# Kernel optimization log

Hardware: AMD Instinct MI355X
Metric: run time of the kernel (lower is better)

Reference implementation:

```python
import jax, jax.numpy as jnp
import numpy as np

N_NODES = 100000
N_EDGES = 1600000
IN_DIM = 128
HID = 64
OUT = 1


def setup_inputs() -> dict:
    key = jax.random.key(0)
    ks = jax.random.split(key, 8)
    x = jax.random.normal(ks[0], (N_NODES, IN_DIM), dtype=jnp.float32)
    edge_src = jax.random.randint(ks[1], (N_EDGES,), 0, N_NODES)
    edge_dst = jax.random.randint(ks[2], (N_EDGES,), 0, N_NODES)
    edge_weight = jax.random.uniform(ks[3], (N_EDGES,), dtype=jnp.float32)
    W1 = jax.random.normal(ks[4], (IN_DIM, HID), dtype=jnp.float32) / np.sqrt(IN_DIM)
    b1 = jnp.zeros((HID,), dtype=jnp.float32)
    W2 = jax.random.normal(ks[5], (HID, OUT), dtype=jnp.float32) / np.sqrt(HID)
    b2 = jnp.zeros((OUT,), dtype=jnp.float32)
    return {"x": x, "edge_src": edge_src, "edge_dst": edge_dst,
            "edge_weight": edge_weight, "W1": W1, "b1": b1, "W2": W2, "b2": b2}


def _spmm(edge_src, edge_dst, edge_weight, h):
    # adj_norm @ h: gather source rows, scale by edge weight, scatter-add to dst
    msgs = edge_weight[:, None] * h[edge_src]           # [E, D]
    return jax.ops.segment_sum(msgs, edge_dst, num_segments=N_NODES)


def reference(x, edge_src, edge_dst, edge_weight, W1, b1, W2, b2):
    # Layer 1: Linear -> SpMM -> relu (dropout is identity in eval mode)
    h = x @ W1 + b1                                      # [N, HID]
    h = _spmm(edge_src, edge_dst, edge_weight, h)
    h = jax.nn.relu(h)
    # Layer 2: Linear -> SpMM (no activation on final layer)
    h = h @ W2 + b2                                      # [N, OUT]
    h = _spmm(edge_src, edge_dst, edge_weight, h)
    return h
```

## Files before the change

kernel.cpp:

```cpp
#include <hip/hip_runtime.h>

#define IN_DIM 128
#define HID 64
#define SHIFT 8
#define BNODES 256
#define NBMAX 1024
#define CH 4096
#define SRCMASK 0xFFFFF
#define LDSCAP 6144
#define XSTR 130

using bf16x8 = __attribute__((ext_vector_type(8))) short;
using f32x4  = __attribute__((ext_vector_type(4))) float;
using f32x2  = __attribute__((ext_vector_type(2))) float;

__device__ inline unsigned short f2bf(float f) {
  unsigned u = __float_as_uint(f);
  u += 0x7FFF + ((u >> 16) & 1);
  return (unsigned short)(u >> 16);
}
__device__ inline float bf2f_lo(unsigned v) {
  return __uint_as_float(v << 16);
}
__device__ inline float bf2f_hi(unsigned v) {
  return __uint_as_float(v & 0xFFFF0000u);
}
__device__ inline f32x2 unpk2(unsigned v) {
  return (f32x2){bf2f_lo(v), bf2f_hi(v)};
}

__device__ inline int xcd_chunk(int bid, int nch) {
  int q = nch >> 3, r = nch & 7;
  int xcd = bid & 7, idx = bid >> 3;
  return (xcd < r) ? xcd * (q + 1) + idx : r * (q + 1) + (xcd - r) * q + idx;
}

__global__ __launch_bounds__(256) void w1pack_kernel(
    const float* __restrict__ W1, unsigned short* __restrict__ W1b,
    int* __restrict__ bucket_size, int NB) {
  if (blockIdx.x == 0) {
    for (int i = threadIdx.x; i < NB; i += 256) bucket_size[i] = 0;
  }
  int idx = blockIdx.x * 256 + threadIdx.x;
  if (idx >= 4 * 4 * 64 * 8) return;
  int i    = idx & 7;
  int lane = (idx >> 3) & 63;
  int kc   = (idx >> 9) & 3;
  int jt   = idx >> 11;
  int k = kc * 32 + ((lane >> 4) << 3) + i;
  int n = jt * 16 + (lane & 15);
  W1b[idx] = f2bf(W1[k * HID + n]);
}

__global__ __launch_bounds__(256) void gemm1_kernel(
    const float* __restrict__ x, const unsigned short* __restrict__ W1b,
    const float* __restrict__ b1, unsigned short* __restrict__ h1, int N) {
  __shared__ unsigned short Xs[4][16][XSTR];
  const int lane = threadIdx.x & 63;
  const int w    = threadIdx.x >> 6;
  const int rblk = blockIdx.x * 64;

  for (int it = 0; it < 8; ++it) {
    int flat = it * 64 + lane;
    int row  = flat >> 5;
    int c4   = (flat & 31) * 4;
    int gr = rblk + w * 16 + row;
    if (gr > N - 1) gr = N - 1;
    float4 v = *reinterpret_cast<const float4*>(x + (long)gr * IN_DIM + c4);
    ushort4 o;
    o.x = f2bf(v.x); o.y = f2bf(v.y); o.z = f2bf(v.z); o.w = f2bf(v.w);
    *reinterpret_cast<ushort4*>(&Xs[w][row][c4]) = o;
  }
  __syncthreads();

  bf16x8 a[4];
#pragma unroll
  for (int kc = 0; kc < 4; ++kc) {
    a[kc] = *reinterpret_cast<const bf16x8*>(
        &Xs[w][lane & 15][kc * 32 + ((lane >> 4) << 3)]);
  }

  const uint4* wb = reinterpret_cast<const uint4*>(W1b);
#pragma unroll
  for (int jt = 0; jt < 4; ++jt) {
    f32x4 acc = {0.f, 0.f, 0.f, 0.f};
#pragma unroll
    for (int kc = 0; kc < 4; ++kc) {
      union { uint4 q; bf16x8 v; } bu;
      bu.q = wb[(jt * 4 + kc) * 64 + lane];
      acc = __builtin_amdgcn_mfma_f32_16x16x32_bf16(a[kc], bu.v, acc, 0, 0, 0);
    }
    const int col = jt * 16 + (lane & 15);
    const float bb = b1[col];
#pragma unroll
    for (int r = 0; r < 4; ++r) {
      int row = (lane >> 4) * 4 + r;
      int gr = rblk + w * 16 + row;
      if (gr < N) h1[(long)gr * HID + col] = f2bf(acc[r] + bb);
    }
  }
}

__global__ __launch_bounds__(512) void bucket_count_kernel(
    const int* __restrict__ dst, int* __restrict__ bucket_size,
    int* __restrict__ blockRel, int NB, int E, int NCH) {
  __shared__ int hist[NBMAX];
  const int c = xcd_chunk(blockIdx.x, NCH);
  for (int i = threadIdx.x; i < NB; i += 512) hist[i] = 0;
  __syncthreads();
  int base = c * CH;
  int end = min(base + CH, E);
  for (int k = base + threadIdx.x * 4; k + 3 < end; k += 2048) {
    int4 d4 = *reinterpret_cast<const int4*>(&dst[k]);
    atomicAdd(&hist[d4.x >> SHIFT], 1);
    atomicAdd(&hist[d4.y >> SHIFT], 1);
    atomicAdd(&hist[d4.z >> SHIFT], 1);
    atomicAdd(&hist[d4.w >> SHIFT], 1);
  }
  int tail_start = base + ((end - base) & ~3);
  for (int k = tail_start + threadIdx.x; k < end; k += 512)
    atomicAdd(&hist[dst[k] >> SHIFT], 1);
  __syncthreads();
  for (int i = threadIdx.x; i < NB; i += 512) {
    int cv = hist[i];
    int r = cv ? atomicAdd(&bucket_size[i], cv) : 0;
    blockRel[(long)c * NB + i] = r;
  }
}

__global__ __launch_bounds__(1024) void bucket_scan_kernel(
    const int* __restrict__ bucket_size, int* __restrict__ bucket_offs, int NB) {
  __shared__ int tmp[1024];
  int tid = threadIdx.x;
  int v = (tid < NB) ? bucket_size[tid] : 0;
  tmp[tid] = v;
  __syncthreads();
  for (int off = 1; off < 1024; off <<= 1) {
    int t = (tid >= off) ? tmp[tid - off] : 0;
    __syncthreads();
    tmp[tid] += t;
    __syncthreads();
  }
  if (tid <= NB) bucket_offs[tid] = tmp[tid] - v;
}

__global__ __launch_bounds__(512) void bucket_place_kernel(
    const int* __restrict__ src, const int* __restrict__ dst,
    const float* __restrict__ w, const int* __restrict__ bucket_offs,
    const int* __restrict__ blockRel, int2* __restrict__ bpart,
    int NB, int E, int NCH) {
  __shared__ int cur[NBMAX];
  const int c = xcd_chunk(blockIdx.x, NCH);
  for (int i = threadIdx.x; i < NB; i += 512)
    cur[i] = bucket_offs[i] + blockRel[(long)c * NB + i];
  __syncthreads();
  int base = c * CH;
  int end = min(base + CH, E);
  for (int k = base + threadIdx.x * 4; k + 3 < end; k += 2048) {
    int4   s4 = *reinterpret_cast<const int4*>(&src[k]);
    int4   d4 = *reinterpret_cast<const int4*>(&dst[k]);
    float4 w4 = *reinterpret_cast<const float4*>(&w[k]);
    int p0 = atomicAdd(&cur[d4.x >> SHIFT], 1);
    int p1 = atomicAdd(&cur[d4.y >> SHIFT], 1);
    int p2 = atomicAdd(&cur[d4.z >> SHIFT], 1);
    int p3 = atomicAdd(&cur[d4.w >> SHIFT], 1);
    bpart[p0] = make_int2((s4.x & SRCMASK) | ((d4.x & (BNODES - 1)) << 20),
                          __float_as_int(w4.x));
    bpart[p1] = make_int2((s4.y & SRCMASK) | ((d4.y & (BNODES - 1)) << 20),
                          __float_as_int(w4.y));
    bpart[p2] = make_int2((s4.z & SRCMASK) | ((d4.z & (BNODES - 1)) << 20),
                          __float_as_int(w4.z));
    bpart[p3] = make_int2((s4.w & SRCMASK) | ((d4.w & (BNODES - 1)) << 20),
                          __float_as_int(w4.w));
  }
  int tail_start = base + ((end - base) & ~3);
  for (int k = tail_start + threadIdx.x; k < end; k += 512) {
    int d = dst[k];
    int b = d >> SHIFT;
    int pos = atomicAdd(&cur[b], 1);
    bpart[pos] = make_int2((src[k] & SRCMASK) | ((d & (BNODES - 1)) << 20),
                           __float_as_int(w[k]));
  }
}

__global__ __launch_bounds__(1024) void csr_place_kernel(
    const int2* __restrict__ bpart, const int* __restrict__ bucket_offs,
    int2* __restrict__ csr, int* __restrict__ noffs, int N, int NB, int E) {
  __shared__ int cnt[BNODES];
  __shared__ int cur[BNODES];
  __shared__ int wtot[4];
  __shared__ int2 ebuf[LDSCAP];
  const int t = threadIdx.x;
  const int b = blockIdx.x;
  const int beg = bucket_offs[b], end = bucket_offs[b + 1];
  const int len = end - beg;
  const bool useLds = (len <= LDSCAP);

  if (t < BNODES) cnt[t] = 0;
  __syncthreads();

  if (useLds) {
    for (int k = t; k < len; k += 1024) {
      int2 e = bpart[beg + k];
      ebuf[k] = e;
      atomicAdd(&cnt[e.x >> 20], 1);
    }
  } else {
    for (int k = beg + t; k < end; k += 1024)
      atomicAdd(&cnt[bpart[k].x >> 20], 1);
  }
  __syncthreads();

  int v = (t < BNODES) ? cnt[t] : 0;
  int s = v;
#pragma unroll
  for (int d = 1; d < 64; d <<= 1) {
    int u = __shfl_up(s, d, 64);
    if ((t & 63) >= d) s += u;
  }
  if (t < BNODES && (t & 63) == 63) wtot[t >> 6] = s;
  __syncthreads();
  if (t < BNODES) {
    int base = 0;
    const int wv_ = t >> 6;
    if (wv_ > 0) base += wtot[0];
    if (wv_ > 1) base += wtot[1];
    if (wv_ > 2) base += wtot[2];
    const int g = beg + base + s - v;
    cur[t] = g;
    const int node = (b << SHIFT) + t;
    if (node < N) noffs[node] = g;
  }
  if (b == NB - 1 && t == 0) noffs[N] = E;
  __syncthreads();

  if (useLds) {
    for (int k = t; k < len; k += 1024) {
      int2 e = ebuf[k];
      int pos = atomicAdd(&cur[e.x >> 20], 1);
      csr[pos] = make_int2(e.x & SRCMASK, e.y);
    }
  } else {
    for (int k = beg + t; k < end; k += 1024) {
      int2 e = bpart[k];
      int pos = atomicAdd(&cur[e.x >> 20], 1);
      csr[pos] = make_int2(e.x & SRCMASK, e.y);
    }
  }
}

__global__ __launch_bounds__(256) void spmm1_fused_kernel(
    const int* __restrict__ noffs, const int2* __restrict__ csr,
    const unsigned short* __restrict__ h1, const float* __restrict__ W2,
    const float* __restrict__ b2, float* __restrict__ h3, int N) {
  int wave = (blockIdx.x * 256 + threadIdx.x) >> 6;
  int lane = threadIdx.x & 63;
  if (wave >= N) return;
  int beg = noffs[wave], end = noffs[wave + 1];
  const int e8 = lane >> 3;
  const int l8 = lane & 7;

  f32x2 a01 = {0.f, 0.f}, a23 = {0.f, 0.f};
  f32x2 a45 = {0.f, 0.f}, a67 = {0.f, 0.f};
  int k = beg + e8;

  int2 eA, eB;
  if (k + 8 < end) { eA = csr[k]; eB = csr[k + 8]; }
  while (k + 8 < end) {
    uint4 vA = *reinterpret_cast<const uint4*>(h1 + (long)eA.x * HID + 8 * l8);
    uint4 vB = *reinterpret_cast<const uint4*>(h1 + (long)eB.x * HID + 8 * l8);
    float wA = __int_as_float(eA.y), wB = __int_as_float(eB.y);
    int kn = k + 16;
    if (kn + 8 < end) { eA = csr[kn]; eB = csr[kn + 8]; }
    f32x2 wA2 = {wA, wA}, wB2 = {wB, wB};
    a01 += wA2 * unpk2(vA.x);
    a23 += wA2 * unpk2(vA.y);
    a45 += wA2 * unpk2(vA.z);
    a67 += wA2 * unpk2(vA.w);
    a01 += wB2 * unpk2(vB.x);
    a23 += wB2 * unpk2(vB.y);
    a45 += wB2 * unpk2(vB.z);
    a67 += wB2 * unpk2(vB.w);
    k = kn;
  }
  for (; k < end; k += 8) {
    int2 e = csr[k];
    uint4 v = *reinterpret_cast<const uint4*>(h1 + (long)e.x * HID + 8 * l8);
    float w = __int_as_float(e.y);
    f32x2 w2v = {w, w};
    a01 += w2v * unpk2(v.x);
    a23 += w2v * unpk2(v.y);
    a45 += w2v * unpk2(v.z);
    a67 += w2v * unpk2(v.w);
  }

  float a0 = a01[0], a1 = a01[1], a2 = a23[0], a3 = a23[1];
  float a4 = a45[0], a5 = a45[1], a6 = a67[0], a7 = a67[1];

  {
    const bool hi = (e8 & 1);
    float s0 = hi ? a0 : a4;  float r0 = __shfl_xor(s0, 8, 64);
    float s1 = hi ? a1 : a5;  float r1 = __shfl_xor(s1, 8, 64);
    float s2 = hi ? a2 : a6;  float r2 = __shfl_xor(s2, 8, 64);
    float s3 = hi ? a3 : a7;  float r3 = __shfl_xor(s3, 8, 64);
    a0 = (hi ? a4 : a0) + r0;
    a1 = (hi ? a5 : a1) + r1;
    a2 = (hi ? a6 : a2) + r2;
    a3 = (hi ? a7 : a3) + r3;
  }
  {
    const bool hi = (e8 >> 1) & 1;
    float s0 = hi ? a0 : a2;  float r0 = __shfl_xor(s0, 16, 64);
    float s1 = hi ? a1 : a3;  float r1 = __shfl_xor(s1, 16, 64);
    a0 = (hi ? a2 : a0) + r0;
    a1 = (hi ? a3 : a1) + r1;
  }
  {
    const bool hi = (e8 >> 2) & 1;
    float s0 = hi ? a0 : a1;  float r0 = __shfl_xor(s0, 32, 64);
    a0 = (hi ? a1 : a0) + r0;
  }
  const int dim = 8 * l8 + 4 * (e8 & 1) + 2 * ((e8 >> 1) & 1) + ((e8 >> 2) & 1);
  float s = fmaxf(a0, 0.f) * W2[dim];
  s += __shfl_xor(s, 1, 64);
  s += __shfl_xor(s, 2, 64);
  s += __shfl_xor(s, 4, 64);
  s += __shfl_xor(s, 8, 64);
  s += __shfl_xor(s, 16, 64);
  s += __shfl_xor(s, 32, 64);
  if (lane == 0) h3[wave] = s + b2[0];
}

__global__ __launch_bounds__(256) void spmm2_gather_kernel(
    const int* __restrict__ noffs, const int2* __restrict__ csr,
    const float* __restrict__ h3, float* __restrict__ out, int N) {
  int n = blockIdx.x * 256 + threadIdx.x;
  if (n >= N) return;
  int beg = noffs[n], end = noffs[n + 1];
  float acc = 0.f;
  int k = beg;
  if (k < end && (k & 1)) {
    int2 e = csr[k];
    acc += __int_as_float(e.y) * h3[e.x];
    ++k;
  }
  for (; k + 1 < end; k += 2) {
    int4 e2 = *reinterpret_cast<const int4*>(&csr[k]);
    acc += __int_as_float(e2.y) * h3[e2.x];
    acc += __int_as_float(e2.w) * h3[e2.z];
  }
  if (k < end) {
    int2 e = csr[k];
    acc += __int_as_float(e.y) * h3[e.x];
  }
  out[n] = acc;
}

extern "C" void kernel_launch(void* const* d_in, const int* in_sizes, int n_in,
                              void* d_out, int out_size, void* d_ws, size_t ws_size,
                              hipStream_t stream) {
  const float* x    = (const float*)d_in[0];
  const int*   esrc = (const int*)d_in[1];
  const int*   edst = (const int*)d_in[2];
  const float* ew   = (const float*)d_in[3];
  const float* W1   = (const float*)d_in[4];
  const float* b1   = (const float*)d_in[5];
  const float* W2   = (const float*)d_in[6];
  const float* b2   = (const float*)d_in[7];
  float* out = (float*)d_out;

  const int N = in_sizes[0] / IN_DIM;
  const int E = in_sizes[1];
  const int NB = (N + BNODES - 1) >> SHIFT;
  const int NCH = (E + CH - 1) / CH;

  char* p = (char*)d_ws;
  auto alloc = [&](size_t bytes) {
    char* r = p;
    p += (bytes + 15) & ~(size_t)15;
    return r;
  };
  unsigned short* h1 = (unsigned short*)alloc((size_t)N * HID * sizeof(unsigned short));
  unsigned short* W1b= (unsigned short*)alloc((size_t)8192 * sizeof(unsigned short));
  float* h3          = (float*)alloc((size_t)N * sizeof(float));
  int*   bucket_size = (int*)alloc((size_t)NB * sizeof(int));
  int*   bucket_offs = (int*)alloc((size_t)(NB + 1) * sizeof(int));
  int*   noffs       = (int*)alloc((size_t)(N + 1) * sizeof(int));
  int*   blockRel    = (int*)alloc((size_t)NCH * NB * sizeof(int));
  int2*  bpart       = (int2*)alloc((size_t)E * sizeof(int2));
  int2*  csr         = (int2*)alloc((size_t)E * sizeof(int2));

  w1pack_kernel<<<32, 256, 0, stream>>>(W1, W1b, bucket_size, NB);
  gemm1_kernel<<<(N + 63) / 64, 256, 0, stream>>>(x, W1b, b1, h1, N);

  bucket_count_kernel<<<NCH, 512, 0, stream>>>(edst, bucket_size, blockRel, NB, E, NCH);
  bucket_scan_kernel<<<1, 1024, 0, stream>>>(bucket_size, bucket_offs, NB);
  bucket_place_kernel<<<NCH, 512, 0, stream>>>(esrc, edst, ew, bucket_offs,
                                               blockRel, bpart, NB, E, NCH);
  csr_place_kernel<<<NB, 1024, 0, stream>>>(bpart, bucket_offs, csr, noffs, N, NB, E);

  spmm1_fused_kernel<<<(unsigned)(((long)N * 64 + 255) / 256), 256, 0, stream>>>(
      noffs, csr, h1, W2, b2, h3, N);

  spmm2_gather_kernel<<<(N + 255) / 256, 256, 0, stream>>>(noffs, csr, h3, out, N);
}
```

Measured before the change: 116.3 us.

## Fuse bucket scan into place kernel; use 8 lanes per node in SpMM2

The standalone single-block bucket prefix-scan kernel is removed. Each bucket_place block now recomputes the bucket offsets with a wave-shuffle scan over at most 512 buckets, and block 0 writes them out for later kernels, which saves a launch and a serial dependency. The second SpMM gather changes from one thread per node to eight lanes per node that stride the edge list and combine with xor-shuffles. This should improve load balance and memory parallelism, at the cost of more threads and dropping the paired int4 loads. The fused scan assumes NB <= 512, which holds here (391 buckets).

```diff
diff --git a/kernel.cpp b/kernel.cpp
--- a/kernel.cpp
+++ b/kernel.cpp
@@ -128,35 +128,41 @@
   }
 }
 
-__global__ __launch_bounds__(1024) void bucket_scan_kernel(
-    const int* __restrict__ bucket_size, int* __restrict__ bucket_offs, int NB) {
-  __shared__ int tmp[1024];
-  int tid = threadIdx.x;
-  int v = (tid < NB) ? bucket_size[tid] : 0;
-  tmp[tid] = v;
-  __syncthreads();
-  for (int off = 1; off < 1024; off <<= 1) {
-    int t = (tid >= off) ? tmp[tid - off] : 0;
-    __syncthreads();
-    tmp[tid] += t;
-    __syncthreads();
-  }
-  if (tid <= NB) bucket_offs[tid] = tmp[tid] - v;
-}
-
 __global__ __launch_bounds__(512) void bucket_place_kernel(
     const int* __restrict__ src, const int* __restrict__ dst,
-    const float* __restrict__ w, const int* __restrict__ bucket_offs,
-    const int* __restrict__ blockRel, int2* __restrict__ bpart,
-    int NB, int E, int NCH) {
+    const float* __restrict__ w, const int* __restrict__ bucket_size,
+    const int* __restrict__ blockRel, int* __restrict__ bucket_offs,
+    int2* __restrict__ bpart, int NB, int E, int NCH) {
   __shared__ int cur[NBMAX];
+  __shared__ int wtot[8];
+  const int t = threadIdx.x;
   const int c = xcd_chunk(blockIdx.x, NCH);
-  for (int i = threadIdx.x; i < NB; i += 512)
-    cur[i] = bucket_offs[i] + blockRel[(long)c * NB + i];
-  __syncthreads();
+
+  int v = (t < NB) ? bucket_size[t] : 0;
+  int s = v;
+#pragma unroll
+  for (int d = 1; d < 64; d <<= 1) {
+    int u = __shfl_up(s, d, 64);
+    if ((t & 63) >= d) s += u;
+  }
+  if ((t & 63) == 63) wtot[t >> 6] = s;
+  __syncthreads();
+  int basew = 0;
+  const int wv_ = t >> 6;
+#pragma unroll
+  for (int i = 0; i < 7; ++i)
+    if (wv_ > i) basew += wtot[i];
+  const int offs = basew + s - v;
+  if (t < NB) {
+    cur[t] = offs + blockRel[(long)c * NB + t];
+    if (blockIdx.x == 0) bucket_offs[t] = offs;
+  }
+  if (blockIdx.x == 0 && t == 0) bucket_offs[NB] = E;
+  __syncthreads();
+
   int base = c * CH;
   int end = min(base + CH, E);
-  for (int k = base + threadIdx.x * 4; k + 3 < end; k += 2048) {
+  for (int k = base + t * 4; k + 3 < end; k += 2048) {
     int4   s4 = *reinterpret_cast<const int4*>(&src[k]);
     int4   d4 = *reinterpret_cast<const int4*>(&dst[k]);
     float4 w4 = *reinterpret_cast<const float4*>(&w[k]);
@@ -174,7 +180,7 @@
                           __float_as_int(w4.w));
   }
   int tail_start = base + ((end - base) & ~3);
-  for (int k = tail_start + threadIdx.x; k < end; k += 512) {
+  for (int k = tail_start + t; k < end; k += 512) {
     int d = dst[k];
     int b = d >> SHIFT;
     int pos = atomicAdd(&cur[b], 1);
@@ -334,26 +340,19 @@
 __global__ __launch_bounds__(256) void spmm2_gather_kernel(
     const int* __restrict__ noffs, const int2* __restrict__ csr,
     const float* __restrict__ h3, float* __restrict__ out, int N) {
-  int n = blockIdx.x * 256 + threadIdx.x;
-  if (n >= N) return;
-  int beg = noffs[n], end = noffs[n + 1];
+  int gid = (blockIdx.x * 256 + threadIdx.x) >> 3;
+  int l8  = threadIdx.x & 7;
+  if (gid >= N) return;
+  int beg = noffs[gid], end = noffs[gid + 1];
   float acc = 0.f;
-  int k = beg;
-  if (k < end && (k & 1)) {
+  for (int k = beg + l8; k < end; k += 8) {
     int2 e = csr[k];
     acc += __int_as_float(e.y) * h3[e.x];
-    ++k;
-  }
-  for (; k + 1 < end; k += 2) {
-    int4 e2 = *reinterpret_cast<const int4*>(&csr[k]);
-    acc += __int_as_float(e2.y) * h3[e2.x];
-    acc += __int_as_float(e2.w) * h3[e2.z];
-  }
-  if (k < end) {
-    int2 e = csr[k];
-    acc += __int_as_float(e.y) * h3[e.x];
-  }
-  out[n] = acc;
+  }
+  acc += __shfl_xor(acc, 1, 64);
+  acc += __shfl_xor(acc, 2, 64);
+  acc += __shfl_xor(acc, 4, 64);
+  if (l8 == 0) out[gid] = acc;
 }
 
 extern "C" void kernel_launch(void* const* d_in, const int* in_sizes, int n_in,
@@ -394,13 +393,14 @@
   gemm1_kernel<<<(N + 63) / 64, 256, 0, stream>>>(x, W1b, b1, h1, N);
 
   bucket_count_kernel<<<NCH, 512, 0, stream>>>(edst, bucket_size, blockRel, NB, E, NCH);
-  bucket_scan_kernel<<<1, 1024, 0, stream>>>(bucket_size, bucket_offs, NB);
-  bucket_place_kernel<<<NCH, 512, 0, stream>>>(esrc, edst, ew, bucket_offs,
-                                               blockRel, bpart, NB, E, NCH);
+  bucket_place_kernel<<<NCH, 512, 0, stream>>>(esrc, edst, ew, bucket_size,
+                                               blockRel, bucket_offs, bpart,
+                                               NB, E, NCH);
   csr_place_kernel<<<NB, 1024, 0, stream>>>(bpart, bucket_offs, csr, noffs, N, NB, E);
 
   spmm1_fused_kernel<<<(unsigned)(((long)N * 64 + 255) / 256), 256, 0, stream>>>(
       noffs, csr, h1, W2, b2, h3, N);
 
-  spmm2_gather_kernel<<<(N + 255) / 256, 256, 0, stream>>>(noffs, csr, h3, out, N);
-}
+  spmm2_gather_kernel<<<(unsigned)(((long)N * 8 + 255) / 256), 256, 0, stream>>>(
+      noffs, csr, h3, out, N);
+}
```

Result: faster. 111.3 us (-4.2%).
